# Kernel tuning notes

Measured on AMD Instinct MI355X. Metric: run time of the kernel, lower is better.

## Reference

```python
import jax, jax.numpy as jnp
import numpy as np

IN_F = 3072
OUT_F = 3072
SCALE = 1.0
KRON_SIZES = (16, 16, 12)  # q1*q2*q3 == IN_F


def setup_inputs() -> dict:
    key = jax.random.key(0)
    ks = jax.random.split(key, 8)
    x = jax.random.normal(ks[0], (4, 4096, IN_F), dtype=jnp.float32)
    # SVD factors of the frozen linear weight (k = min(out, in) = 3072)
    U = jax.random.normal(ks[1], (OUT_F, OUT_F), dtype=jnp.float32) * 0.02
    S = jax.random.uniform(ks[2], (OUT_F,), dtype=jnp.float32)  # nonnegative singular values
    V = jax.random.normal(ks[3], (OUT_F, IN_F), dtype=jnp.float32) * 0.02
    delta = jnp.full((OUT_F,), 0.001, dtype=jnp.float32)
    q1, q2, q3 = KRON_SIZES
    # initialized as identity in the module; add tiny noise so grads are nontrivial
    Q1 = jnp.eye(q1, dtype=jnp.float32) + 0.01 * jax.random.normal(ks[4], (q1, q1), dtype=jnp.float32)
    Q2 = jnp.eye(q2, dtype=jnp.float32) + 0.01 * jax.random.normal(ks[5], (q2, q2), dtype=jnp.float32)
    Q3 = jnp.eye(q3, dtype=jnp.float32) + 0.01 * jax.random.normal(ks[6], (q3, q3), dtype=jnp.float32)
    return {"x": x, "U": U, "S": S, "V": V, "delta": delta, "Q1": Q1, "Q2": Q2, "Q3": Q3}


def reference(x, U, S, V, delta, Q1, Q2, Q3):
    # S' = relu(S + delta); W = U @ diag(S') @ V  (diag fused as column scaling)
    Sp = jax.nn.relu(S + delta)
    W = (U * Sp[None, :]) @ V                      # [out, in]
    ortho = jnp.kron(jnp.kron(Q1, Q2), Q3)         # [in, in]
    W_t = ortho @ W.T                              # [in, out]
    # F.linear(input, W_t.t()) == input @ W_t ; dropout_p = 0 (inference)
    out = jnp.einsum('bsd,do->bso', x, W_t)
    return out * SCALE
```

## Files before the change

### kernel.cpp

```cpp
#include <hip/hip_runtime.h>

typedef unsigned short u16;
typedef unsigned int u32;
typedef __attribute__((ext_vector_type(8))) __bf16 bf16x8;
typedef __attribute__((ext_vector_type(4))) float f32x4;
typedef __attribute__((ext_vector_type(8))) u16 u16x8;


__device__ __forceinline__ u16 f2bf(float f) {
    union { float f; u32 u; } v; v.f = f;
    u32 r = v.u + 0x7FFFu + ((v.u >> 16) & 1u);
    return (u16)(r >> 16);
}

__device__ __forceinline__ void gload16(const void* g, void* l) {
    __builtin_amdgcn_global_load_lds(
        (const __attribute__((address_space(1))) u32*)g,
        (__attribute__((address_space(3))) u32*)l,
        16, 0, 0);
}

__global__ __launch_bounds__(256) void conv_bf16(
    const float* __restrict__ in, u16* __restrict__ out) {
    const size_t i = (size_t)blockIdx.x * 256 + threadIdx.x;
    const float4 a = ((const float4*)in)[i * 2];
    const float4 b = ((const float4*)in)[i * 2 + 1];
    u16x8 o;
    o[0] = f2bf(a.x); o[1] = f2bf(a.y); o[2] = f2bf(a.z); o[3] = f2bf(a.w);
    o[4] = f2bf(b.x); o[5] = f2bf(b.y); o[6] = f2bf(b.z); o[7] = f2bf(b.w);
    ((u16x8*)out)[i] = o;
}

__global__ __launch_bounds__(64) void conv_scale(
    const float* __restrict__ U, const float* __restrict__ S,
    const float* __restrict__ D, u16* __restrict__ out) {
    const int m = blockIdx.y;
    const int k = (blockIdx.x * 64 + threadIdx.x) * 8;
    const size_t base = (size_t)m * 3072 + k;
    const float4 a = *(const float4*)&U[base];
    const float4 b = *(const float4*)&U[base + 4];
    const float4 s1 = *(const float4*)&S[k], s2 = *(const float4*)&S[k + 4];
    const float4 d1 = *(const float4*)&D[k], d2 = *(const float4*)&D[k + 4];
    u16x8 o;
    o[0] = f2bf(a.x * fmaxf(s1.x + d1.x, 0.f));
    o[1] = f2bf(a.y * fmaxf(s1.y + d1.y, 0.f));
    o[2] = f2bf(a.z * fmaxf(s1.z + d1.z, 0.f));
    o[3] = f2bf(a.w * fmaxf(s1.w + d1.w, 0.f));
    o[4] = f2bf(b.x * fmaxf(s2.x + d2.x, 0.f));
    o[5] = f2bf(b.y * fmaxf(s2.y + d2.y, 0.f));
    o[6] = f2bf(b.z * fmaxf(s2.z + d2.z, 0.f));
    o[7] = f2bf(b.w * fmaxf(s2.w + d2.w, 0.f));
    *(u16x8*)&out[base] = o;
}

__global__ __launch_bounds__(256) void transpose_conv(
    const float* __restrict__ V, u16* __restrict__ Vt, int n) {
    __shared__ float tile[64][65];
    const int k0 = blockIdx.y * 64, j0 = blockIdx.x * 64;
    const int t = threadIdx.x;
    const int r = t >> 4, c4 = t & 15;
#pragma unroll
    for (int i = 0; i < 4; i++) {
        int row = i * 16 + r;
        const float4 v = *(const float4*)&V[(size_t)(k0 + row) * n + j0 + c4 * 4];
        tile[row][c4 * 4 + 0] = v.x;
        tile[row][c4 * 4 + 1] = v.y;
        tile[row][c4 * 4 + 2] = v.z;
        tile[row][c4 * 4 + 3] = v.w;
    }
    __syncthreads();
#pragma unroll
    for (int i = 0; i < 4; i++) {
        int row = i * 16 + r;
        ushort4 o;
        o.x = f2bf(tile[c4 * 4 + 0][row]);
        o.y = f2bf(tile[c4 * 4 + 1][row]);
        o.z = f2bf(tile[c4 * 4 + 2][row]);
        o.w = f2bf(tile[c4 * 4 + 3][row]);
        *(ushort4*)&Vt[(size_t)(j0 + row) * n + k0 + c4 * 4] = o;
    }
}

__global__ __launch_bounds__(256) void gemm_bt(
    const u16* __restrict__ A, const u16* __restrict__ B,
    float* __restrict__ C, int M, int N, int K) {
    __shared__ u16 As[128 * 64];
    __shared__ u16 Bs[128 * 64];
    const int t = threadIdx.x;
    const int m0 = blockIdx.y * 128, n0 = blockIdx.x * 128;
    const int wave = t >> 6, lane = t & 63;
    const int quad = lane >> 4, lrow = lane & 15;
    const int wm = (wave >> 1) * 64, wn = (wave & 1) * 64;
    const int gr = t >> 3;
    const int gc = (t & 7) ^ (gr & 7);
    const int c0 = (quad ^ (lrow & 7)) * 8;
    f32x4 acc[4][4] = {};

    const u16* Ag = A + (size_t)(m0 + gr) * K + gc * 8;
    const u16* Bg = B + (size_t)(n0 + gr) * K + gc * 8;

    for (int kb = 0; kb < K; kb += 64) {
#pragma unroll
        for (int i = 0; i < 4; i++) {
            gload16(Ag + (size_t)i * 32 * K + kb, (char*)As + i * 4096 + t * 16);
            gload16(Bg + (size_t)i * 32 * K + kb, (char*)Bs + i * 4096 + t * 16);
        }
        __syncthreads();
#pragma unroll
        for (int kk = 0; kk < 2; kk++) {
            const int co = c0 ^ (kk * 32);
            bf16x8 af[4], bfr[4];
#pragma unroll
            for (int mi = 0; mi < 4; mi++)
                af[mi] = *(const bf16x8*)&As[(wm + mi * 16 + lrow) * 64 + co];
#pragma unroll
            for (int ni = 0; ni < 4; ni++)
                bfr[ni] = *(const bf16x8*)&Bs[(wn + ni * 16 + lrow) * 64 + co];
#pragma unroll
            for (int mi = 0; mi < 4; mi++)
#pragma unroll
                for (int ni = 0; ni < 4; ni++)
                    acc[mi][ni] = __builtin_amdgcn_mfma_f32_16x16x32_bf16(
                        af[mi], bfr[ni], acc[mi][ni], 0, 0, 0);
        }
        __syncthreads();
    }
#pragma unroll
    for (int mi = 0; mi < 4; mi++) {
#pragma unroll
        for (int rr = 0; rr < 4; rr++) {
            int row = m0 + wm + mi * 16 + quad * 4 + rr;
            float* cp = C + (size_t)row * N + n0 + wn + lrow;
#pragma unroll
            for (int ni = 0; ni < 4; ni++) cp[ni * 16] = acc[mi][ni][rr];
        }
    }
}

__global__ __launch_bounds__(256) void kron_apply(
    const float* __restrict__ W, const float* __restrict__ Q1,
    const float* __restrict__ Q2, const float* __restrict__ Q3,
    u16* __restrict__ WtT) {
    __shared__ float T0[3072], T1[3072];
    __shared__ float Q1s[256], Q2s[256], Q3s[144];
    const int o = blockIdx.x, t = threadIdx.x;
#pragma unroll
    for (int i = 0; i < 12; i++) T0[t + i * 256] = W[(size_t)o * 3072 + t + i * 256];
    Q1s[t] = Q1[t];
    Q2s[t] = Q2[t];
    if (t < 144) Q3s[t] = Q3[t];
    __syncthreads();
#pragma unroll
    for (int i = 0; i < 12; i++) {
        int e = t + i * 256;
        int d1 = e / 192, rem = e % 192;
        float s = 0.f;
#pragma unroll
        for (int j1 = 0; j1 < 16; j1++) s += Q1s[d1 * 16 + j1] * T0[j1 * 192 + rem];
        T1[e] = s;
    }
    __syncthreads();
#pragma unroll
    for (int i = 0; i < 12; i++) {
        int e = t + i * 256;
        int j3 = e % 12, d2 = (e / 12) & 15, d1 = e / 192;
        float s = 0.f;
#pragma unroll
        for (int j2 = 0; j2 < 16; j2++) s += Q2s[d2 * 16 + j2] * T1[d1 * 192 + j2 * 12 + j3];
        T0[e] = s;
    }
    __syncthreads();
#pragma unroll
    for (int i = 0; i < 12; i++) {
        int e = t + i * 256;
        int d3 = e % 12, b = e - d3;
        float s = 0.f;
#pragma unroll
        for (int j3 = 0; j3 < 12; j3++) s += Q3s[d3 * 12 + j3] * T0[b + j3];
        WtT[(size_t)o * 3072 + e] = f2bf(s);
    }
}

extern "C" void kernel_launch(void* const* d_in, const int* in_sizes, int n_in,
                              void* d_out, int out_size, void* d_ws, size_t ws_size,
                              hipStream_t stream) {
    const float* x   = (const float*)d_in[0];
    const float* U   = (const float*)d_in[1];
    const float* S   = (const float*)d_in[2];
    const float* V   = (const float*)d_in[3];
    const float* dl  = (const float*)d_in[4];
    const float* Q1  = (const float*)d_in[5];
    const float* Q2  = (const float*)d_in[6];
    const float* Q3  = (const float*)d_in[7];
    float* out = (float*)d_out;

    char* ws = (char*)d_ws;
    u16*   xb  = (u16*)ws;
    u16*   Ub  = (u16*)(ws + 100663296);
    u16*   Vt  = (u16*)(ws + 100663296 + 18874368);
    float* W   = (float*)(ws + 100663296 + 2 * 18874368);
    u16*   WtT = Ub;

    hipLaunchKernelGGL(conv_bf16, dim3(24576), dim3(256), 0, stream, x, xb);
    hipLaunchKernelGGL(conv_scale, dim3(6, 3072), dim3(64), 0, stream, U, S, dl, Ub);
    hipLaunchKernelGGL(transpose_conv, dim3(48, 48), dim3(256), 0, stream, V, Vt, 3072);
    hipLaunchKernelGGL(gemm_bt, dim3(24, 24), dim3(256), 0, stream,
                       Ub, Vt, W, 3072, 3072, 3072);
    hipLaunchKernelGGL(kron_apply, dim3(3072), dim3(256), 0, stream, W, Q1, Q2, Q3, WtT);
    hipLaunchKernelGGL(gemm_bt, dim3(24, 128), dim3(256), 0, stream,
                       xb, WtT, out, 16384, 3072, 3072);
}
```

Measured before the change: 959.2 us.

## Replace main activation GEMM with 256x256 pipelined 8-wave kernel

Adds a new GEMM kernel with 256x256 output tiles and 512 threads. It double-buffers LDS in 32-wide K halves and interleaves global-to-LDS prefetch with MFMA phases. It raises MFMA priority with setprio and remaps block IDs so neighbouring tiles share cache across 8 groups. The large x @ W_t GEMM switches to it to cut the exposed global-load latency and the per-tile overhead of the old single-buffered 128x128 kernel. In exchange it needs more registers and LDS, and its hand-tuned waitcnt counts must match the number of in-flight loads exactly.

```diff
diff --git a/kernel.cpp b/kernel.cpp
--- a/kernel.cpp
+++ b/kernel.cpp
@@ -137,6 +137,140 @@
     }
 }
 
+__global__ __launch_bounds__(512, 2) void gemm256(
+    const u16* __restrict__ A, const u16* __restrict__ B,
+    float* __restrict__ C, int M, int N, int K) {
+    __shared__ u16 As[2][2][8192];
+    __shared__ u16 Bs[2][2][8192];
+    const int t = threadIdx.x;
+
+    const int nbx = gridDim.x;
+    const int bid = blockIdx.y * nbx + blockIdx.x;
+    const int cpx = (nbx * gridDim.y) >> 3;
+    const int sid = (bid & 7) * cpx + (bid >> 3);
+    const int m0 = (sid / nbx) * 256, n0 = (sid % nbx) * 256;
+
+    const int lane = t & 63, quad = lane >> 4, lrow = lane & 15;
+    const int wave = t >> 6, wr = wave >> 2, wc = wave & 3;
+
+    const u16* Ag = A + (size_t)(m0 + (t >> 2)) * K + (t & 3) * 8;
+    const u16* Bg = B + (size_t)(n0 + (t >> 2)) * K + (t & 3) * 8;
+    const size_t row128 = (size_t)128 * K;
+
+    const int aoff = (wr * 128 + lrow) * 32 + quad * 8;
+    const int boff = (wc * 64 + lrow) * 32 + quad * 8;
+
+    f32x4 acc[8][4] = {};
+
+#define STG(Gp, RG, kb, kh) do {                                              \
+        gload16((Gp) + (kb) + (kh) * 32, (char*)(RG) + t * 16);               \
+        gload16((Gp) + row128 + (kb) + (kh) * 32, (char*)(RG) + 8192 + t * 16); \
+    } while (0)
+
+    STG(Ag, As[0][0], 0, 0);
+    STG(Bg, Bs[0][0], 0, 0);
+    STG(Ag, As[0][1], 0, 1);
+    STG(Bg, Bs[0][1], 0, 1);
+    STG(Ag, As[1][0], 64, 0);
+    STG(Bg, Bs[1][0], 64, 0);
+    asm volatile("s_waitcnt vmcnt(4)" ::: "memory");
+    __builtin_amdgcn_s_barrier();
+
+    const int NT = K >> 6;
+    for (int tt = 0; tt < NT; ++tt) {
+        const int b = tt & 1;
+        const u16* A0 = As[b][0];
+        const u16* A1 = As[b][1];
+        const u16* B0 = Bs[b][0];
+        const u16* B1 = Bs[b][1];
+        bf16x8 bq[4], aq[4];
+
+#pragma unroll
+        for (int ni = 0; ni < 4; ni++) bq[ni] = *(const bf16x8*)&B0[boff + ni * 512];
+#pragma unroll
+        for (int mi = 0; mi < 4; mi++) aq[mi] = *(const bf16x8*)&A0[aoff + mi * 512];
+        if (tt + 1 < NT) STG(Ag, As[b ^ 1][1], (tt + 1) * 64, 1);
+        __builtin_amdgcn_s_barrier();
+        asm volatile("s_waitcnt lgkmcnt(0)" ::: "memory");
+        __builtin_amdgcn_sched_barrier(0);
+        __builtin_amdgcn_s_setprio(1);
+#pragma unroll
+        for (int mi = 0; mi < 4; mi++)
+#pragma unroll
+            for (int ni = 0; ni < 4; ni++)
+                acc[mi][ni] = __builtin_amdgcn_mfma_f32_16x16x32_bf16(
+                    aq[mi], bq[ni], acc[mi][ni], 0, 0, 0);
+        __builtin_amdgcn_s_setprio(0);
+        __builtin_amdgcn_s_barrier();
+
+#pragma unroll
+        for (int mi = 0; mi < 4; mi++) aq[mi] = *(const bf16x8*)&A0[aoff + (mi + 4) * 512];
+        if (tt + 1 < NT) STG(Bg, Bs[b ^ 1][1], (tt + 1) * 64, 1);
+        __builtin_amdgcn_s_barrier();
+        asm volatile("s_waitcnt lgkmcnt(0)" ::: "memory");
+        __builtin_amdgcn_sched_barrier(0);
+        __builtin_amdgcn_s_setprio(1);
+#pragma unroll
+        for (int mi = 0; mi < 4; mi++)
+#pragma unroll
+            for (int ni = 0; ni < 4; ni++)
+                acc[mi + 4][ni] = __builtin_amdgcn_mfma_f32_16x16x32_bf16(
+                    aq[mi], bq[ni], acc[mi + 4][ni], 0, 0, 0);
+        __builtin_amdgcn_s_setprio(0);
+        __builtin_amdgcn_s_barrier();
+
+#pragma unroll
+        for (int ni = 0; ni < 4; ni++) bq[ni] = *(const bf16x8*)&B1[boff + ni * 512];
+#pragma unroll
+        for (int mi = 0; mi < 4; mi++) aq[mi] = *(const bf16x8*)&A1[aoff + mi * 512];
+        if (tt + 2 < NT) STG(Ag, As[b][0], (tt + 2) * 64, 0);
+        __builtin_amdgcn_s_barrier();
+        asm volatile("s_waitcnt lgkmcnt(0)" ::: "memory");
+        __builtin_amdgcn_sched_barrier(0);
+        __builtin_amdgcn_s_setprio(1);
+#pragma unroll
+        for (int mi = 0; mi < 4; mi++)
+#pragma unroll
+            for (int ni = 0; ni < 4; ni++)
+                acc[mi][ni] = __builtin_amdgcn_mfma_f32_16x16x32_bf16(
+                    aq[mi], bq[ni], acc[mi][ni], 0, 0, 0);
+        __builtin_amdgcn_s_setprio(0);
+        __builtin_amdgcn_s_barrier();
+
+#pragma unroll
+        for (int mi = 0; mi < 4; mi++) aq[mi] = *(const bf16x8*)&A1[aoff + (mi + 4) * 512];
+        if (tt + 2 < NT) STG(Bg, Bs[b][0], (tt + 2) * 64, 0);
+        __builtin_amdgcn_s_barrier();
+        asm volatile("s_waitcnt lgkmcnt(0)" ::: "memory");
+        __builtin_amdgcn_sched_barrier(0);
+        __builtin_amdgcn_s_setprio(1);
+#pragma unroll
+        for (int mi = 0; mi < 4; mi++)
+#pragma unroll
+            for (int ni = 0; ni < 4; ni++)
+                acc[mi + 4][ni] = __builtin_amdgcn_mfma_f32_16x16x32_bf16(
+                    aq[mi], bq[ni], acc[mi + 4][ni], 0, 0, 0);
+        __builtin_amdgcn_s_setprio(0);
+        if (tt + 2 < NT)
+            asm volatile("s_waitcnt vmcnt(4)" ::: "memory");
+        else if (tt + 1 < NT)
+            asm volatile("s_waitcnt vmcnt(0)" ::: "memory");
+        __builtin_amdgcn_s_barrier();
+    }
+#undef STG
+
+#pragma unroll
+    for (int mi = 0; mi < 8; mi++) {
+#pragma unroll
+        for (int rr = 0; rr < 4; rr++) {
+            const int row = m0 + wr * 128 + mi * 16 + quad * 4 + rr;
+            float* cp = C + (size_t)row * N + n0 + wc * 64 + lrow;
+#pragma unroll
+            for (int ni = 0; ni < 4; ni++) cp[ni * 16] = acc[mi][ni][rr];
+        }
+    }
+}
+
 __global__ __launch_bounds__(256) void kron_apply(
     const float* __restrict__ W, const float* __restrict__ Q1,
     const float* __restrict__ Q2, const float* __restrict__ Q3,
@@ -207,6 +341,6 @@
     hipLaunchKernelGGL(gemm_bt, dim3(24, 24), dim3(256), 0, stream,
                        Ub, Vt, W, 3072, 3072, 3072);
     hipLaunchKernelGGL(kron_apply, dim3(3072), dim3(256), 0, stream, W, Q1, Q2, Q3, WtT);
-    hipLaunchKernelGGL(gemm_bt, dim3(24, 128), dim3(256), 0, stream,
+    hipLaunchKernelGGL(gemm256, dim3(12, 64), dim3(512), 0, stream,
                        xb, WtT, out, 16384, 3072, 3072);
 }
```

After: 838.1 us. 12.6% less time.

## Replace GEMM with 256x256-tile double-buffered, phase-interleaved MFMA kernel

Applied to the files above, without the earlier changes.

Replaces the 128x128 single-buffered GEMM with a 512-thread, 256x256-tile kernel that double-buffers LDS and splits each K-step into four phases. Global-to-LDS loads for the next tiles are interleaved with MFMA work using explicit waitcnt, barriers and setprio. It also remaps block IDs into XCD-grouped chunks for cache locality and uses a new LDS swizzle. This is meant to hide global load latency and raise data reuse per tile, at the cost of 128KB of LDS per block, more registers and fragile hand-tuned sync.

```diff
diff --git a/kernel.cpp b/kernel.cpp
--- a/kernel.cpp
+++ b/kernel.cpp
@@ -81,56 +81,112 @@
     }
 }
 
-__global__ __launch_bounds__(256) void gemm_bt(
+__global__ __launch_bounds__(512, 2) void gemm256(
     const u16* __restrict__ A, const u16* __restrict__ B,
     float* __restrict__ C, int M, int N, int K) {
-    __shared__ u16 As[128 * 64];
-    __shared__ u16 Bs[128 * 64];
+    __shared__ u16 As[2][16384];
+    __shared__ u16 Bs[2][16384];
     const int t = threadIdx.x;
-    const int m0 = blockIdx.y * 128, n0 = blockIdx.x * 128;
-    const int wave = t >> 6, lane = t & 63;
-    const int quad = lane >> 4, lrow = lane & 15;
-    const int wm = (wave >> 1) * 64, wn = (wave & 1) * 64;
-    const int gr = t >> 3;
-    const int gc = (t & 7) ^ (gr & 7);
-    const int c0 = (quad ^ (lrow & 7)) * 8;
-    f32x4 acc[4][4] = {};
-
-    const u16* Ag = A + (size_t)(m0 + gr) * K + gc * 8;
-    const u16* Bg = B + (size_t)(n0 + gr) * K + gc * 8;
-
-    for (int kb = 0; kb < K; kb += 64) {
-#pragma unroll
-        for (int i = 0; i < 4; i++) {
-            gload16(Ag + (size_t)i * 32 * K + kb, (char*)As + i * 4096 + t * 16);
-            gload16(Bg + (size_t)i * 32 * K + kb, (char*)Bs + i * 4096 + t * 16);
+
+    const int nbx = gridDim.x;
+    const int bid = blockIdx.y * nbx + blockIdx.x;
+    const int cpx = (nbx * gridDim.y) >> 3;
+    const int sid = (bid & 7) * cpx + (bid >> 3);
+    const int m0 = (sid / nbx) * 256, n0 = (sid % nbx) * 256;
+
+    const int lane = t & 63, quad = lane >> 4, lrow = lane & 15;
+    const int wave = t >> 6, wr = wave >> 2, wc = wave & 3;
+
+    const int schunk = (t & 7) ^ ((t >> 4) & 2);
+    const u16* Ag = A + (size_t)(m0 + (t >> 3)) * K + schunk * 8;
+    const u16* Bg = B + (size_t)(n0 + (t >> 3)) * K + schunk * 8;
+
+    const int swzq = quad ^ ((lrow >> 1) & 2);
+    const int aoff = (wr * 128 + lrow) * 64 + swzq * 8;
+    const int boff = (wc * 64 + lrow) * 64 + swzq * 8;
+
+    f32x4 acc[8][4] = {};
+
+#define STGA(dst, q, kbe) gload16(Ag + (size_t)(q) * 64 * K + (kbe), (char*)(dst) + (q) * 8192 + t * 16)
+#define STGB(dst, q, kbe) gload16(Bg + (size_t)(q) * 64 * K + (kbe), (char*)(dst) + (q) * 8192 + t * 16)
+
+    const int NT = K >> 6;
+    STGA(As[0], 0, 0); STGA(As[0], 1, 0); STGA(As[0], 2, 0); STGA(As[0], 3, 0);
+    STGB(Bs[0], 0, 0); STGB(Bs[0], 1, 0); STGB(Bs[0], 2, 0); STGB(Bs[0], 3, 0);
+    if (NT > 1) {
+        STGA(As[1], 0, 64); STGA(As[1], 2, 64);
+        STGB(Bs[1], 0, 64); STGB(Bs[1], 1, 64);
+        asm volatile("s_waitcnt vmcnt(4)" ::: "memory");
+    } else {
+        asm volatile("s_waitcnt vmcnt(0)" ::: "memory");
+    }
+    __builtin_amdgcn_s_barrier();
+
+    for (int tt = 0; tt < NT; ++tt) {
+        const int b = tt & 1;
+        const u16* Acur = As[b];
+        const u16* Bcur = Bs[b];
+        u16* Anxt = As[b ^ 1];
+        u16* Bnxt = Bs[b ^ 1];
+        bf16x8 bq[4], aq[4];
+
+#define PHASE_TAIL(OFF)                                                       \
+        __builtin_amdgcn_s_barrier();                                         \
+        asm volatile("s_waitcnt lgkmcnt(0)" ::: "memory");                    \
+        __builtin_amdgcn_sched_barrier(0);                                    \
+        __builtin_amdgcn_s_setprio(1);                                        \
+        _Pragma("unroll")                                                     \
+        for (int mi = 0; mi < 4; mi++)                                        \
+            _Pragma("unroll")                                                 \
+            for (int ni = 0; ni < 4; ni++)                                    \
+                acc[mi + OFF][ni] = __builtin_amdgcn_mfma_f32_16x16x32_bf16(  \
+                    aq[mi], bq[ni], acc[mi + OFF][ni], 0, 0, 0);              \
+        __builtin_amdgcn_s_setprio(0);
+
+#pragma unroll
+        for (int ni = 0; ni < 4; ni++) bq[ni] = *(const bf16x8*)&Bcur[boff + ni * 1024];
+#pragma unroll
+        for (int mi = 0; mi < 4; mi++) aq[mi] = *(const bf16x8*)&Acur[aoff + mi * 1024];
+        if (tt + 1 < NT) { STGA(Anxt, 1, (tt + 1) * 64); STGA(Anxt, 3, (tt + 1) * 64); }
+        PHASE_TAIL(0)
+        __builtin_amdgcn_s_barrier();
+
+#pragma unroll
+        for (int mi = 0; mi < 4; mi++) aq[mi] = *(const bf16x8*)&Acur[aoff + (mi + 4) * 1024];
+        if (tt + 1 < NT) { STGB(Bnxt, 2, (tt + 1) * 64); STGB(Bnxt, 3, (tt + 1) * 64); }
+        PHASE_TAIL(4)
+        __builtin_amdgcn_s_barrier();
+
+#pragma unroll
+        for (int ni = 0; ni < 4; ni++) bq[ni] = *(const bf16x8*)&Bcur[boff + ni * 1024 + 32];
+#pragma unroll
+        for (int mi = 0; mi < 4; mi++) aq[mi] = *(const bf16x8*)&Acur[aoff + mi * 1024 + 32];
+        PHASE_TAIL(0)
+        __builtin_amdgcn_s_barrier();
+
+#pragma unroll
+        for (int mi = 0; mi < 4; mi++) aq[mi] = *(const bf16x8*)&Acur[aoff + (mi + 4) * 1024 + 32];
+        if (tt + 2 < NT) {
+            STGA((u16*)Acur, 0, (tt + 2) * 64); STGA((u16*)Acur, 2, (tt + 2) * 64);
+            STGB((u16*)Bcur, 0, (tt + 2) * 64); STGB((u16*)Bcur, 1, (tt + 2) * 64);
         }
-        __syncthreads();
-#pragma unroll
-        for (int kk = 0; kk < 2; kk++) {
-            const int co = c0 ^ (kk * 32);
-            bf16x8 af[4], bfr[4];
-#pragma unroll
-            for (int mi = 0; mi < 4; mi++)
-                af[mi] = *(const bf16x8*)&As[(wm + mi * 16 + lrow) * 64 + co];
-#pragma unroll
-            for (int ni = 0; ni < 4; ni++)
-                bfr[ni] = *(const bf16x8*)&Bs[(wn + ni * 16 + lrow) * 64 + co];
-#pragma unroll
-            for (int mi = 0; mi < 4; mi++)
-#pragma unroll
-                for (int ni = 0; ni < 4; ni++)
-                    acc[mi][ni] = __builtin_amdgcn_mfma_f32_16x16x32_bf16(
-                        af[mi], bfr[ni], acc[mi][ni], 0, 0, 0);
-        }
-        __syncthreads();
-    }
-#pragma unroll
-    for (int mi = 0; mi < 4; mi++) {
+        PHASE_TAIL(4)
+        if (tt + 2 < NT)
+            asm volatile("s_waitcnt vmcnt(4)" ::: "memory");
+        else
+            asm volatile("s_waitcnt vmcnt(0)" ::: "memory");
+        __builtin_amdgcn_s_barrier();
+#undef PHASE_TAIL
+    }
+#undef STGA
+#undef STGB
+
+#pragma unroll
+    for (int mi = 0; mi < 8; mi++) {
 #pragma unroll
         for (int rr = 0; rr < 4; rr++) {
-            int row = m0 + wm + mi * 16 + quad * 4 + rr;
-            float* cp = C + (size_t)row * N + n0 + wn + lrow;
+            const int row = m0 + wr * 128 + mi * 16 + quad * 4 + rr;
+            float* cp = C + (size_t)row * N + n0 + wc * 64 + lrow;
 #pragma unroll
             for (int ni = 0; ni < 4; ni++) cp[ni * 16] = acc[mi][ni][rr];
         }
@@ -204,9 +260,9 @@
     hipLaunchKernelGGL(conv_bf16, dim3(24576), dim3(256), 0, stream, x, xb);
     hipLaunchKernelGGL(conv_scale, dim3(6, 3072), dim3(64), 0, stream, U, S, dl, Ub);
     hipLaunchKernelGGL(transpose_conv, dim3(48, 48), dim3(256), 0, stream, V, Vt, 3072);
-    hipLaunchKernelGGL(gemm_bt, dim3(24, 24), dim3(256), 0, stream,
+    hipLaunchKernelGGL(gemm256, dim3(12, 12), dim3(512), 0, stream,
                        Ub, Vt, W, 3072, 3072, 3072);
     hipLaunchKernelGGL(kron_apply, dim3(3072), dim3(256), 0, stream, W, Q1, Q2, Q3, WtT);
-    hipLaunchKernelGGL(gemm_bt, dim3(24, 128), dim3(256), 0, stream,
+    hipLaunchKernelGGL(gemm256, dim3(12, 64), dim3(512), 0, stream,
                        xb, WtT, out, 16384, 3072, 3072);
 }
```

Result: faster. 873.1 us (-9.0%).
